# Optimization experiments

Measured on AMD Instinct MI355X. Metric: run time of the kernel, lower is better.

## Reference

```python
import jax, jax.numpy as jnp
import numpy as np

IN, H, OUT = 512, 1024, 256
ODE_UNFOLDS = 6
EPS = 1e-08


def setup_inputs() -> dict:
    key = jax.random.key(0)
    ks = jax.random.split(key, 12)
    B, S = 64, 256
    inp = {
        "x": jax.random.normal(ks[0], (B, S, IN), dtype=jnp.float32),
        "h0": jnp.zeros((B, H), dtype=jnp.float32),
        "timespans": jnp.ones((B, S), dtype=jnp.float32),
        # parameters (nn.Linear default-style init scales)
        "tau": jax.random.uniform(ks[1], (H,), minval=1.0, maxval=100.0, dtype=jnp.float32),
        "W_in_w": jax.random.normal(ks[2], (H, IN), dtype=jnp.float32) / np.sqrt(IN),
        "W_in_b": jax.random.normal(ks[3], (H,), dtype=jnp.float32) / np.sqrt(IN),
        "W_rec_w": jax.random.normal(ks[4], (H, H), dtype=jnp.float32) / np.sqrt(H),
        "wiring_mask": jnp.ones((H, H), dtype=jnp.float32),  # AUTO_NCP -> else branch -> ones
        "W_out_w": jax.random.normal(ks[5], (OUT, H), dtype=jnp.float32) / np.sqrt(H),
        "W_out_b": jax.random.normal(ks[6], (OUT,), dtype=jnp.float32) / np.sqrt(H),
        "alpha": jnp.ones((H,), dtype=jnp.float32) * 0.9,
        "beta": jnp.ones((H,), dtype=jnp.float32),
        "mu": jnp.zeros((H,), dtype=jnp.float32),
        "sigma": jnp.ones((H,), dtype=jnp.float32),
    }
    return inp


def reference(x, h0, timespans, tau, W_in_w, W_in_b, W_rec_w, wiring_mask,
              W_out_w, W_out_b, alpha, beta, mu, sigma):
    # masked recurrent weight (constant across time, hoisted out of the loop)
    w_rec = W_rec_w * wiring_mask  # (H, H)

    def time_step(h, inp):
        x_t, dt = inp  # x_t: (B, IN), dt: (B, 1)
        i_in = x_t @ W_in_w.T + W_in_b  # constant across unfolds for this t
        d = dt / ODE_UNFOLDS

        def unfold(h, _):
            i_rec = h @ w_rec.T  # (B, H)
            f = jax.nn.sigmoid((i_rec - mu) / (sigma + EPS))
            dhdt = -alpha * h + beta * f * (i_in + i_rec)
            return h + d * dhdt / tau, None

        h, _ = jax.lax.scan(unfold, h, None, length=ODE_UNFOLDS)
        y_t = h @ W_out_w.T + W_out_b  # (B, OUT)
        return h, y_t

    xs = (jnp.swapaxes(x, 0, 1), jnp.swapaxes(timespans, 0, 1)[..., None])  # (S,B,IN),(S,B,1)
    h_final, ys = jax.lax.scan(time_step, h0, xs)  # ys: (S, B, OUT)
    output = jnp.swapaxes(ys, 0, 1)  # (B, S, OUT)
    return output, h_final
```

## Files before the change

### kernel.cpp

```cpp
#include <hip/hip_runtime.h>

#define IN_DIM   512
#define H_DIM    1024
#define OUT_DIM  256
#define B_DIM    64
#define S_DIM    256
#define EPS_F    1e-8f

#define BPG      4
#define JPW      64
#define NTHREADS 512
#define NWG      256
#define SLOT_STRIDE 65536

#define OUT_Y_TOTAL ((size_t)B_DIM*S_DIM*OUT_DIM)

typedef float    f32x4 __attribute__((ext_vector_type(4)));
typedef unsigned u32x4 __attribute__((ext_vector_type(4)));
typedef short    s16x8 __attribute__((ext_vector_type(8)));

#define MFMA16 __builtin_amdgcn_mfma_f32_16x16x32_bf16

union B8 { unsigned u[4]; s16x8 v; };

__device__ __forceinline__ s16x8 round_bf16x8(f32x4 f0, f32x4 f1) {
  B8 H;
  float fv[8];
#pragma unroll
  for (int e = 0; e < 4; ++e) { fv[e] = f0[e]; fv[e+4] = f1[e]; }
#pragma unroll
  for (int d = 0; d < 4; ++d) {
    unsigned u0 = __float_as_uint(fv[2*d])   + 0x8000u;
    unsigned u1 = __float_as_uint(fv[2*d+1]) + 0x8000u;
    H.u[d] = (u0 >> 16) | (u1 & 0xFFFF0000u);
  }
  return H.v;
}

__device__ __forceinline__ void split_bf16(f32x4 f0, f32x4 f1, s16x8* hi, s16x8* lo) {
  B8 H, L;
  float fv[8];
#pragma unroll
  for (int e = 0; e < 4; ++e) { fv[e] = f0[e]; fv[e+4] = f1[e]; }
#pragma unroll
  for (int d = 0; d < 4; ++d) {
    unsigned u0 = __float_as_uint(fv[2*d]);
    unsigned u1 = __float_as_uint(fv[2*d+1]);
    unsigned t0 = u0 & 0xffff0000u, t1 = u1 & 0xffff0000u;
    H.u[d] = (u0 >> 16) | t1;
    L.u[d] = ((__float_as_uint(fv[2*d]   - __uint_as_float(t0))) >> 16)
           | ((__float_as_uint(fv[2*d+1] - __uint_as_float(t1))) & 0xffff0000u);
  }
  *hi = H.v; *lo = L.v;
}

__device__ __forceinline__ unsigned dec_tag(u32x4 q) {
  return (q.x & 7u) | ((q.y & 7u) << 3) | ((q.z & 7u) << 6) | ((q.w & 7u) << 9);
}
__device__ __forceinline__ s16x8 pack_hi(u32x4 a, u32x4 b) {
  B8 t;
  t.u[0] = (a.y & 0xFFFF0000u) | (a.x >> 16);
  t.u[1] = (a.w & 0xFFFF0000u) | (a.z >> 16);
  t.u[2] = (b.y & 0xFFFF0000u) | (b.x >> 16);
  t.u[3] = (b.w & 0xFFFF0000u) | (b.z >> 16);
  return t.v;
}
__device__ __forceinline__ s16x8 pack_lo(u32x4 a, u32x4 b) {
  B8 t;
  t.u[0] = ((a.y & 0xFFF8u) << 16) | (a.x & 0xFFF8u);
  t.u[1] = ((a.w & 0xFFF8u) << 16) | (a.z & 0xFFF8u);
  t.u[2] = ((b.y & 0xFFF8u) << 16) | (b.x & 0xFFF8u);
  t.u[3] = ((b.w & 0xFFF8u) << 16) | (b.z & 0xFFF8u);
  return t.v;
}

__global__ void __launch_bounds__(NTHREADS)
ltc_kernel(const float* __restrict__ x, const float* __restrict__ h0,
           const float* __restrict__ tspan, const float* __restrict__ tau,
           const float* __restrict__ Wiw, const float* __restrict__ Wib,
           const float* __restrict__ Wrw, const float* __restrict__ wmask,
           const float* __restrict__ Wow, const float* __restrict__ Wob,
           const float* __restrict__ alpha_p, const float* __restrict__ beta_p,
           const float* __restrict__ mu_p, const float* __restrict__ sigma_p,
           float* __restrict__ out, unsigned* __restrict__ hb)
{
  __shared__ float sch[2][8][4][68];
  __shared__ float scx[8][4][68];
  __shared__ float scy[8][4][20];
  __shared__ __align__(16) char winlds[65536];

  const int tid = threadIdx.x;
  const int wg  = blockIdx.x;
  const int g   = wg >> 4;
  const int w   = wg & 15;
  const int b0g = g * BPG;
  const int jw0 = w * JPW;
  const int l   = tid & 63;
  const int v   = tid >> 6;
  const int vb  = v & 3;
  const int gb_e = b0g + vb;
  const int gj  = jw0 + l;

  s16x8 wbh[4][4];
#pragma unroll
  for (int i = 0; i < 4; ++i) {
    const int k0 = v*128 + i*32 + ((l >> 4) << 3);
#pragma unroll
    for (int nt = 0; nt < 4; ++nt) {
      const size_t go = (size_t)(jw0 + nt*16 + (l & 15))*H_DIM + k0;
      f32x4 w0 = *(const f32x4*)(Wrw + go)     * *(const f32x4*)(wmask + go);
      f32x4 w1 = *(const f32x4*)(Wrw + go + 4) * *(const f32x4*)(wmask + go + 4);
      wbh[i][nt] = round_bf16x8(w0, w1);
    }
  }

#pragma unroll
  for (int i2 = 0; i2 < 2; ++i2)
#pragma unroll
    for (int nt = 0; nt < 4; ++nt) {
      const float* wp = Wiw + (size_t)(jw0 + nt*16 + (l & 15))*IN_DIM
                      + v*64 + i2*32 + ((l >> 4) << 3);
      s16x8 wh = round_bf16x8(*(const f32x4*)wp, *(const f32x4*)(wp + 4));
      *(s16x8*)(winlds + ((v*2 + i2)*4 + nt)*1024 + l*16) = wh;
    }

  const float mu_s  = mu_p[gj];
  const float sgi_s = 1.0f / (sigma_p[gj] + EPS_F);
  const float al_s  = alpha_p[gj];
  const float be_s  = beta_p[gj];
  const float ti_s  = 1.0f / tau[gj];
  const float wib_s = Wib[gj];
  float hold_s = h0[((size_t)gb_e << 10) + gj];
  float tsc = tspan[(size_t)gb_e*S_DIM] * (1.0f/6.0f);

  auto store_h = [&](float hn, unsigned slot, unsigned tag) {
    unsigned uh = __float_as_uint(hn) & 0xFFFF0000u;
    float r = hn - __uint_as_float(uh);
    unsigned e = (uh | (__float_as_uint(r) >> 16)) & ~7u;
    e |= (tag >> (3*(l & 3))) & 7u;
    unsigned* dst = hb + slot*SLOT_STRIDE + ((unsigned)gb_e << 10) + (unsigned)gj;
    asm volatile("global_store_dword %0, %1, off sc0 sc1"
                 :: "v"(dst), "v"(e) : "memory");
  };

  if (v < 4) store_h(hold_s, 0u, 0u);

  auto acquire = [&](unsigned slotC, unsigned tagC,
                     u32x4& q0, u32x4& q1, u32x4& q2, u32x4& q3,
                     u32x4& q4, u32x4& q5, u32x4& q6, u32x4& q7) {
    const unsigned* ap = hb + slotC*SLOT_STRIDE
                       + ((unsigned)(b0g + (l & 15)) << 10)
                       + (unsigned)(v*128 + ((l >> 4) << 3));
    for (;;) {
      int ok;
      if ((l & 15) < 4) {
        asm volatile(
          "global_load_dwordx4 %0, %2, off sc0 sc1\n\t"
          "global_load_dwordx4 %1, %2, off offset:256 sc0 sc1\n\t"
          "s_waitcnt vmcnt(0)"
          : "=&v"(q0), "=&v"(q4) : "v"(ap) : "memory");
        ok = (dec_tag(q0) == tagC) & (dec_tag(q4) == tagC);
      } else ok = 1;
      if (__all(ok)) break;
      __builtin_amdgcn_s_sleep(1);
    }
    for (;;) {
      int ok;
      if ((l & 15) < 4) {
        asm volatile(
          "global_load_dwordx4 %0, %6, off offset:16 sc0 sc1\n\t"
          "global_load_dwordx4 %1, %6, off offset:128 sc0 sc1\n\t"
          "global_load_dwordx4 %2, %6, off offset:144 sc0 sc1\n\t"
          "global_load_dwordx4 %3, %6, off offset:272 sc0 sc1\n\t"
          "global_load_dwordx4 %4, %6, off offset:384 sc0 sc1\n\t"
          "global_load_dwordx4 %5, %6, off offset:400 sc0 sc1\n\t"
          "s_waitcnt vmcnt(0)"
          : "=&v"(q1), "=&v"(q2), "=&v"(q3), "=&v"(q5), "=&v"(q6), "=&v"(q7)
          : "v"(ap) : "memory");
        ok = (dec_tag(q1) == tagC) & (dec_tag(q2) == tagC) & (dec_tag(q3) == tagC) &
             (dec_tag(q5) == tagC) & (dec_tag(q6) == tagC) & (dec_tag(q7) == tagC);
      } else ok = 1;
      if (__all(ok)) break;
      __builtin_amdgcn_s_sleep(1);
    }
  };

  auto iin_partials = [&](int tt, f32x4 ax[4]) {
    const int r = l & 15, c = (l >> 4) << 3;
    const float* xp = x + ((size_t)(b0g + (r & 3))*S_DIM + tt)*IN_DIM + v*64 + c;
    f32x4 xq0 = *(const f32x4*)xp,        xq1 = *(const f32x4*)(xp + 4);
    f32x4 xq2 = *(const f32x4*)(xp + 32), xq3 = *(const f32x4*)(xp + 36);
#pragma unroll
    for (int i2 = 0; i2 < 2; ++i2) {
      s16x8 xh, xl;
      split_bf16(i2 ? xq2 : xq0, i2 ? xq3 : xq1, &xh, &xl);
#pragma unroll
      for (int nt = 0; nt < 4; ++nt) {
        s16x8 wh = *(const s16x8*)(winlds + ((v*2 + i2)*4 + nt)*1024 + l*16);
        ax[nt] = MFMA16(xh, wh, ax[nt], 0,0,0);
        ax[nt] = MFMA16(xl, wh, ax[nt], 0,0,0);
      }
    }
  };

  auto load_wout = [&](s16x8 woY[4]) {
#pragma unroll
    for (int i = 0; i < 4; ++i) {
      const int k0 = v*128 + i*32 + ((l >> 4) << 3);
      const size_t go = (size_t)(w*16 + (l & 15))*H_DIM + k0;
      woY[i] = round_bf16x8(*(const f32x4*)(Wow + go), *(const f32x4*)(Wow + go + 4));
    }
  };

  float iin4 = 0.f, iin_nx = 0.f;
  {
    f32x4 ax[4] = {{0,0,0,0},{0,0,0,0},{0,0,0,0},{0,0,0,0}};
    iin_partials(0, ax);
    if (l < 16) {
#pragma unroll
      for (int nt = 0; nt < 4; ++nt)
#pragma unroll
        for (int q = 0; q < 4; ++q) scx[v][q][nt*16 + l] = ax[nt][q];
    }
    __syncthreads();
    if (v < 4) {
      float s = wib_s;
#pragma unroll
      for (int kp = 0; kp < 8; ++kp) s += scx[kp][vb][l];
      iin4 = s;
    }
    __syncthreads();
  }

  unsigned p = 1;
#pragma unroll 1
  for (int t = 0; t < S_DIM; ++t) {
#pragma unroll 1
    for (int u = 0; u < 6; ++u, ++p) {
      const unsigned slotC = (p-1) & 1, tagC = (p-1) & 0xFFFu;
      const unsigned slotP = p & 1,     tagP = p & 0xFFFu;
      const bool doY = (u == 0);
      const bool doX = (u == 3) && (t + 1 < S_DIM);

      s16x8 woY[4];
      if (doY) load_wout(woY);

      u32x4 q0,q1,q2,q3,q4,q5,q6,q7;
      acquire(slotC, tagC, q0,q1,q2,q3,q4,q5,q6,q7);

      f32x4 acc[4] = {{0,0,0,0},{0,0,0,0},{0,0,0,0},{0,0,0,0}};
      f32x4 accy = {0.f,0.f,0.f,0.f};
#pragma unroll
      for (int i = 0; i < 4; ++i) {
        u32x4 qa = (i==0) ? q0 : (i==1) ? q2 : (i==2) ? q4 : q6;
        u32x4 qb = (i==0) ? q1 : (i==1) ? q3 : (i==2) ? q5 : q7;
        s16x8 ah = pack_hi(qa, qb), al = pack_lo(qa, qb);
#pragma unroll
        for (int nt = 0; nt < 4; ++nt) {
          acc[nt] = MFMA16(ah, wbh[i][nt], acc[nt], 0,0,0);
          acc[nt] = MFMA16(al, wbh[i][nt], acc[nt], 0,0,0);
        }
        if (doY) {
          accy = MFMA16(ah, woY[i], accy, 0,0,0);
          accy = MFMA16(al, woY[i], accy, 0,0,0);
        }
      }
      f32x4 ax[4] = {{0,0,0,0},{0,0,0,0},{0,0,0,0},{0,0,0,0}};
      if (doX) iin_partials(t + 1, ax);

      if (l < 16) {
#pragma unroll
        for (int nt = 0; nt < 4; ++nt)
#pragma unroll
          for (int q = 0; q < 4; ++q) sch[slotP][v][q][nt*16 + l] = acc[nt][q];
        if (doX) {
#pragma unroll
          for (int nt = 0; nt < 4; ++nt)
#pragma unroll
            for (int q = 0; q < 4; ++q) scx[v][q][nt*16 + l] = ax[nt][q];
        }
        if (doY) {
#pragma unroll
          for (int q = 0; q < 4; ++q) scy[v][q][l] = accy[q];
        }
      }
      __syncthreads();

      if (v < 4) {
        float ir = 0.f;
#pragma unroll
        for (int kp = 0; kp < 8; ++kp) ir += sch[slotP][kp][vb][l];
        const float z  = (ir - mu_s) * sgi_s;
        const float f  = 1.0f / (1.0f + __expf(-z));
        const float dh = -al_s*hold_s + be_s*f*(iin4 + ir);
        const float hn = hold_s + tsc*dh*ti_s;
        hold_s = hn;
        store_h(hn, slotP, tagP);
        if (doX) {
          float s = wib_s;
#pragma unroll
          for (int kp = 0; kp < 8; ++kp) s += scx[kp][vb][l];
          iin_nx = s;
        }
        if (u == 5) {
          if (t + 1 < S_DIM) {
            tsc = tspan[(size_t)gb_e*S_DIM + t + 1] * (1.0f/6.0f);
            iin4 = iin_nx;
          } else {
            out[OUT_Y_TOTAL + ((size_t)gb_e << 10) + gj] = hn;
          }
        }
      } else if (v == 4 && doY && t > 0) {
        const int b = l >> 4, oc = l & 15;
        float s = Wob[w*16 + oc];
#pragma unroll
        for (int kp = 0; kp < 8; ++kp) s += scy[kp][b][oc];
        out[((size_t)(b0g + b)*S_DIM + (t-1))*OUT_DIM + w*16 + oc] = s;
      }
    }
  }

  {
    const unsigned slotC = (p-1) & 1, tagC = (p-1) & 0xFFFu;
    s16x8 woY[4];
    load_wout(woY);
    u32x4 q0,q1,q2,q3,q4,q5,q6,q7;
    acquire(slotC, tagC, q0,q1,q2,q3,q4,q5,q6,q7);
    f32x4 accy = {0.f,0.f,0.f,0.f};
#pragma unroll
    for (int i = 0; i < 4; ++i) {
      u32x4 qa = (i==0) ? q0 : (i==1) ? q2 : (i==2) ? q4 : q6;
      u32x4 qb = (i==0) ? q1 : (i==1) ? q3 : (i==2) ? q5 : q7;
      s16x8 ah = pack_hi(qa, qb), al = pack_lo(qa, qb);
      accy = MFMA16(ah, woY[i], accy, 0,0,0);
      accy = MFMA16(al, woY[i], accy, 0,0,0);
    }
    if (l < 16) {
#pragma unroll
      for (int q = 0; q < 4; ++q) scy[v][q][l] = accy[q];
    }
    __syncthreads();
    if (v == 4) {
      const int b = l >> 4, oc = l & 15;
      float s = Wob[w*16 + oc];
#pragma unroll
      for (int kp = 0; kp < 8; ++kp) s += scy[kp][b][oc];
      out[((size_t)(b0g + b)*S_DIM + (S_DIM-1))*OUT_DIM + w*16 + oc] = s;
    }
  }
}

extern "C" void kernel_launch(void* const* d_in, const int* in_sizes, int n_in,
                              void* d_out, int out_size, void* d_ws, size_t ws_size,
                              hipStream_t stream) {
  const float* x    = (const float*)d_in[0];
  const float* h0   = (const float*)d_in[1];
  const float* ts   = (const float*)d_in[2];
  const float* tau  = (const float*)d_in[3];
  const float* Wiw  = (const float*)d_in[4];
  const float* Wib  = (const float*)d_in[5];
  const float* Wrw  = (const float*)d_in[6];
  const float* msk  = (const float*)d_in[7];
  const float* Wow  = (const float*)d_in[8];
  const float* Wob  = (const float*)d_in[9];
  const float* alp  = (const float*)d_in[10];
  const float* bet  = (const float*)d_in[11];
  const float* mu   = (const float*)d_in[12];
  const float* sg   = (const float*)d_in[13];
  float* out = (float*)d_out;
  unsigned* hb = (unsigned*)d_ws;

  hipMemsetAsync(hb, 0xFF, 2*SLOT_STRIDE*sizeof(unsigned), stream);

  void* args[] = { (void*)&x, (void*)&h0, (void*)&ts, (void*)&tau,
                   (void*)&Wiw, (void*)&Wib, (void*)&Wrw, (void*)&msk,
                   (void*)&Wow, (void*)&Wob, (void*)&alp, (void*)&bet,
                   (void*)&mu, (void*)&sg, (void*)&out, (void*)&hb };
  hipLaunchCooperativeKernel((const void*)ltc_kernel, dim3(NWG), dim3(NTHREADS),
                             args, 0, stream);
}
```

Before: 4.756 ms.

## Move off-critical-path Y and input projections after h publish, add single-shot acquire fast path

The output projection (accy) and next-step input projection (ax) are moved after the h update and store, so the new hidden state is published to other workgroups sooner, shortening the cross-workgroup dependency chain. Their reductions are deferred by one unfold (u==1 for Y, u==4 for X) and read from shared scratch written in the prior iteration. Acquire also gains a fast path that issues all eight tagged loads at once before falling back to the staged polling loop. The risk is a race on the scx/scy shared buffers now written after the barrier, and extra load traffic when the data is not yet ready.

```diff
diff --git a/kernel.cpp b/kernel.cpp
--- a/kernel.cpp
+++ b/kernel.cpp
@@ -151,6 +151,29 @@
     const unsigned* ap = hb + slotC*SLOT_STRIDE
                        + ((unsigned)(b0g + (l & 15)) << 10)
                        + (unsigned)(v*128 + ((l >> 4) << 3));
+    {
+      int ok;
+      if ((l & 15) < 4) {
+        asm volatile(
+          "global_load_dwordx4 %0, %8, off sc0 sc1\n\t"
+          "global_load_dwordx4 %1, %8, off offset:16 sc0 sc1\n\t"
+          "global_load_dwordx4 %2, %8, off offset:128 sc0 sc1\n\t"
+          "global_load_dwordx4 %3, %8, off offset:144 sc0 sc1\n\t"
+          "global_load_dwordx4 %4, %8, off offset:256 sc0 sc1\n\t"
+          "global_load_dwordx4 %5, %8, off offset:272 sc0 sc1\n\t"
+          "global_load_dwordx4 %6, %8, off offset:384 sc0 sc1\n\t"
+          "global_load_dwordx4 %7, %8, off offset:400 sc0 sc1\n\t"
+          "s_waitcnt vmcnt(0)"
+          : "=&v"(q0), "=&v"(q1), "=&v"(q2), "=&v"(q3),
+            "=&v"(q4), "=&v"(q5), "=&v"(q6), "=&v"(q7)
+          : "v"(ap) : "memory");
+        ok = (dec_tag(q0) == tagC) & (dec_tag(q1) == tagC) &
+             (dec_tag(q2) == tagC) & (dec_tag(q3) == tagC) &
+             (dec_tag(q4) == tagC) & (dec_tag(q5) == tagC) &
+             (dec_tag(q6) == tagC) & (dec_tag(q7) == tagC);
+      } else ok = 1;
+      if (__all(ok)) return;
+    }
     for (;;) {
       int ok;
       if ((l & 15) < 4) {
@@ -249,7 +272,6 @@
       acquire(slotC, tagC, q0,q1,q2,q3,q4,q5,q6,q7);
 
       f32x4 acc[4] = {{0,0,0,0},{0,0,0,0},{0,0,0,0},{0,0,0,0}};
-      f32x4 accy = {0.f,0.f,0.f,0.f};
 #pragma unroll
       for (int i = 0; i < 4; ++i) {
         u32x4 qa = (i==0) ? q0 : (i==1) ? q2 : (i==2) ? q4 : q6;
@@ -260,29 +282,12 @@
           acc[nt] = MFMA16(ah, wbh[i][nt], acc[nt], 0,0,0);
           acc[nt] = MFMA16(al, wbh[i][nt], acc[nt], 0,0,0);
         }
-        if (doY) {
-          accy = MFMA16(ah, woY[i], accy, 0,0,0);
-          accy = MFMA16(al, woY[i], accy, 0,0,0);
-        }
-      }
-      f32x4 ax[4] = {{0,0,0,0},{0,0,0,0},{0,0,0,0},{0,0,0,0}};
-      if (doX) iin_partials(t + 1, ax);
-
+      }
       if (l < 16) {
 #pragma unroll
         for (int nt = 0; nt < 4; ++nt)
 #pragma unroll
           for (int q = 0; q < 4; ++q) sch[slotP][v][q][nt*16 + l] = acc[nt][q];
-        if (doX) {
-#pragma unroll
-          for (int nt = 0; nt < 4; ++nt)
-#pragma unroll
-            for (int q = 0; q < 4; ++q) scx[v][q][nt*16 + l] = ax[nt][q];
-        }
-        if (doY) {
-#pragma unroll
-          for (int q = 0; q < 4; ++q) scy[v][q][l] = accy[q];
-        }
       }
       __syncthreads();
 
@@ -296,7 +301,7 @@
         const float hn = hold_s + tsc*dh*ti_s;
         hold_s = hn;
         store_h(hn, slotP, tagP);
-        if (doX) {
+        if (u == 4 && t + 1 < S_DIM) {
           float s = wib_s;
 #pragma unroll
           for (int kp = 0; kp < 8; ++kp) s += scx[kp][vb][l];
@@ -310,12 +315,38 @@
             out[OUT_Y_TOTAL + ((size_t)gb_e << 10) + gj] = hn;
           }
         }
-      } else if (v == 4 && doY && t > 0) {
+      } else if (v == 4 && u == 1 && t > 0) {
         const int b = l >> 4, oc = l & 15;
         float s = Wob[w*16 + oc];
 #pragma unroll
         for (int kp = 0; kp < 8; ++kp) s += scy[kp][b][oc];
         out[((size_t)(b0g + b)*S_DIM + (t-1))*OUT_DIM + w*16 + oc] = s;
+      }
+
+      if (doY) {
+        f32x4 accy = {0.f,0.f,0.f,0.f};
+#pragma unroll
+        for (int i = 0; i < 4; ++i) {
+          u32x4 qa = (i==0) ? q0 : (i==1) ? q2 : (i==2) ? q4 : q6;
+          u32x4 qb = (i==0) ? q1 : (i==1) ? q3 : (i==2) ? q5 : q7;
+          s16x8 ah = pack_hi(qa, qb), al = pack_lo(qa, qb);
+          accy = MFMA16(ah, woY[i], accy, 0,0,0);
+          accy = MFMA16(al, woY[i], accy, 0,0,0);
+        }
+        if (l < 16) {
+#pragma unroll
+          for (int q = 0; q < 4; ++q) scy[v][q][l] = accy[q];
+        }
+      }
+      if (doX) {
+        f32x4 ax[4] = {{0,0,0,0},{0,0,0,0},{0,0,0,0},{0,0,0,0}};
+        iin_partials(t + 1, ax);
+        if (l < 16) {
+#pragma unroll
+          for (int nt = 0; nt < 4; ++nt)
+#pragma unroll
+            for (int q = 0; q < 4; ++q) scx[v][q][nt*16 + l] = ax[nt][q];
+        }
       }
     }
   }
```

New measurement: 4.648 ms. 2.3% less time.
